# Optimization experiments

Hardware: AMD Instinct MI355X
Metric: run time of the kernel (lower is better)

## Reference

```python
import jax, jax.numpy as jnp
import numpy as np
import math

H = 12  # heads (init kwarg)
KEEP_RATE = 0.7  # forward arg keep_rate (< 1 -> token pruning path)


def setup_inputs() -> dict:
    key = jax.random.key(0)
    k0, k1, k2 = jax.random.split(key, 3)
    b, n, c = 32, 577, 768  # ViT-B/16 @ 384px: 576 patches + CLS
    x = jax.random.normal(k0, (b, n, c), dtype=jnp.float32)
    # nn.Linear(dim, dim*3) and nn.Linear(dim, dim); kaiming-ish scale
    W_qkv = jax.random.normal(k1, (c, 3 * c), dtype=jnp.float32) / np.sqrt(c).astype(np.float32)
    b_qkv = jnp.zeros((3 * c,), dtype=jnp.float32)
    W_out = jax.random.normal(k2, (c, c), dtype=jnp.float32) / np.sqrt(c).astype(np.float32)
    b_out = jnp.zeros((c,), dtype=jnp.float32)
    return {"x": x, "keep_rate": KEEP_RATE, "W_qkv": W_qkv, "b_qkv": b_qkv,
            "W_out": W_out, "b_out": b_out}


def reference(x, keep_rate, W_qkv, b_qkv, W_out, b_out):
    b, n, c = x.shape
    d = c // H
    scale = (c / H) ** -0.5
    # qkv projection + split into heads: 'b n (h d) -> b h n d'
    qkv = x @ W_qkv + b_qkv                      # [b, n, 3c]
    q, k, v = jnp.split(qkv, 3, axis=-1)
    split_heads = lambda t: t.reshape(b, n, H, d).transpose(0, 2, 1, 3)
    q, k, v = split_heads(q), split_heads(k), split_heads(v)
    dots = jnp.einsum('bhid,bhjd->bhij', q, k) * scale   # [b,h,n,n]
    attention = jax.nn.softmax(dots, axis=-1)
    out = jnp.einsum('bhij,bhjd->bhid', attention, v)    # [b,h,n,d]
    out = out.transpose(0, 2, 1, 3).reshape(b, n, c)     # 'b h n d -> b n (h d)'
    out = out @ W_out + b_out                            # to_out (dropout=0)
    final_tokens = n - 1
    if keep_rate < 1:
        final_tokens = math.ceil(keep_rate * final_tokens)
        # CLS-token attention to patch tokens, averaged over heads
        class_attention = attention[:, :, 0, 1:].mean(axis=1)   # [b, n-1]
        _, ind = jax.lax.top_k(class_attention, final_tokens)    # [b, final_tokens]
        ind = jnp.sort(ind, axis=1)
        index = jnp.broadcast_to(ind[:, :, None], (b, final_tokens, c))
        return (x, index, ind, class_attention, final_tokens)
    return (out, None, None, None, final_tokens)
```

## Files before the change

kernel.cpp:

```cpp
#include <hip/hip_runtime.h>
#include <hip/hip_bf16.h>
#include <math.h>

#define BATCH 32
#define NTOK 577
#define NPATCH 576
#define CDIM 768
#define HEADS 12
#define DHEAD 64
#define W3 2304
#define FT 404

#define WS_WTIL  24576
#define WS_DBIAS 319488
#define WS_DOTS  319872
#define WS_IND   541440

#define O_X      0ULL
#define O_INDEX  14180352ULL
#define O_IND    24109056ULL
#define O_CA     24121984ULL
#define O_FT     24140416ULL

__global__ __launch_bounds__(256) void k_fold(const float* __restrict__ x,
                                              const float* __restrict__ W,
                                              const float* __restrict__ bias,
                                              float* __restrict__ wtil,
                                              float* __restrict__ dbias) {
    __shared__ float x0s[CDIM];
    __shared__ float red[256];
    __shared__ float qs[DHEAD];
    const int b = blockIdx.x, h = blockIdx.y, tid = threadIdx.x;
    for (int i = tid; i < CDIM; i += 256) x0s[i] = x[(size_t)b * NTOK * CDIM + i];
    __syncthreads();
    {
        const int d = tid & 63, seg = tid >> 6;
        const float* Wq = W + (size_t)(h * DHEAD + d);
        float acc = 0.f;
        const int c0 = seg * 192;
        #pragma unroll 8
        for (int c = c0; c < c0 + 192; c++)
            acc += x0s[c] * Wq[(size_t)c * W3];
        red[tid] = acc;
    }
    __syncthreads();
    if (tid < DHEAD) {
        float q = red[tid] + red[tid + 64] + red[tid + 128] + red[tid + 192]
                + bias[h * DHEAD + tid];
        qs[tid] = q;
        float t = q * bias[CDIM + h * DHEAD + tid];
        #pragma unroll
        for (int off = 32; off; off >>= 1) t += __shfl_down(t, off);
        if (tid == 0) dbias[b * HEADS + h] = t;
    }
    __syncthreads();
    for (int c = tid; c < CDIM; c += 256) {
        const float* wr = W + (size_t)c * W3 + CDIM + h * DHEAD;
        float acc = 0.f;
        #pragma unroll
        for (int d = 0; d < DHEAD; d += 4) {
            float4 a = *reinterpret_cast<const float4*>(wr + d);
            acc += a.x * qs[d] + a.y * qs[d + 1] + a.z * qs[d + 2] + a.w * qs[d + 3];
        }
        wtil[((size_t)b * HEADS + h) * CDIM + c] = acc;
    }
}

__global__ __launch_bounds__(256) void k_dots(const float* __restrict__ x,
                                              const float* __restrict__ wtil,
                                              const float* __restrict__ dbias,
                                              float* __restrict__ dots,
                                              float* __restrict__ out0) {
    __shared__ float wt[HEADS * CDIM];
    __shared__ float db[HEADS];
    const int b = blockIdx.x, tid = threadIdx.x;
    for (int i = tid; i < HEADS * CDIM; i += 256) wt[i] = wtil[(size_t)b * HEADS * CDIM + i];
    if (tid < HEADS) db[tid] = dbias[b * HEADS + tid];
    __syncthreads();
    const int wave = tid >> 6, lane = tid & 63;
    for (int it = 0; it < 8; it++) {
        const int j = blockIdx.y * 32 + it * 4 + wave;
        if (j >= NTOK) break;
        const float4* xp = reinterpret_cast<const float4*>(x + ((size_t)b * NTOK + j) * CDIM);
        float4* op = reinterpret_cast<float4*>(out0 + ((size_t)b * NTOK + j) * CDIM);
        float acc[HEADS];
        #pragma unroll
        for (int h = 0; h < HEADS; h++) acc[h] = 0.f;
        #pragma unroll
        for (int i = 0; i < 3; i++) {
            float4 a = xp[i * 64 + lane];
            op[i * 64 + lane] = a;
            const int cbase = i * 256 + lane * 4;
            #pragma unroll
            for (int h = 0; h < HEADS; h++) {
                float4 w = *reinterpret_cast<const float4*>(&wt[h * CDIM + cbase]);
                acc[h] += a.x * w.x + a.y * w.y + a.z * w.z + a.w * w.w;
            }
        }
        #pragma unroll
        for (int off = 32; off; off >>= 1)
            #pragma unroll
            for (int h = 0; h < HEADS; h++) acc[h] += __shfl_xor(acc[h], off);
        if (lane == 0) {
            #pragma unroll
            for (int h = 0; h < HEADS; h++)
                dots[((size_t)b * HEADS + h) * NTOK + j] = 0.125f * (acc[h] + db[h]);
        }
    }
}

__global__ __launch_bounds__(768) void k_catopk(const float* __restrict__ dots,
                                                float* __restrict__ ca_out,
                                                float* __restrict__ ind_out,
                                                float* __restrict__ ft_out,
                                                int* __restrict__ ind_ws,
                                                int write_ft) {
    __shared__ float dl[HEADS * NTOK];
    __shared__ float mh[HEADS], sh[HEADS];
    __shared__ unsigned int vals[NPATCH];
    __shared__ int wsum[12];
    const int b = blockIdx.x, tid = threadIdx.x;
    const int w = tid >> 6, lane = tid & 63;
    for (int i = tid; i < HEADS * NTOK; i += 768) dl[i] = dots[(size_t)b * HEADS * NTOK + i];
    __syncthreads();
    {
        const float* row = dl + w * NTOK;
        float m = -3.4e38f;
        for (int j = lane; j < NTOK; j += 64) m = fmaxf(m, row[j]);
        #pragma unroll
        for (int off = 32; off; off >>= 1) m = fmaxf(m, __shfl_xor(m, off));
        float s = 0.f;
        for (int j = lane; j < NTOK; j += 64) s += expf(row[j] - m);
        #pragma unroll
        for (int off = 32; off; off >>= 1) s += __shfl_xor(s, off);
        if (lane == 0) { mh[w] = m; sh[w] = s; }
    }
    __syncthreads();
    unsigned int myv = 0;
    if (tid < NPATCH) {
        float ca = 0.f;
        #pragma unroll
        for (int h = 0; h < HEADS; h++)
            ca += expf(dl[h * NTOK + 1 + tid] - mh[h]) / sh[h];
        ca *= (1.f / 12.f);
        ca_out[(size_t)b * NPATCH + tid] = ca;
        myv = __float_as_uint(ca);
        vals[tid] = myv;
    }
    __syncthreads();
    int f = 0;
    if (tid < NPATCH) {
        int rank = 0;
        const uint4* v4 = reinterpret_cast<const uint4*>(vals);
        #pragma unroll 4
        for (int jb = 0; jb < NPATCH / 4; jb++) {
            const uint4 v = v4[jb];
            const int j = jb * 4;
            rank += (v.x > myv) || (v.x == myv && (j + 0) < tid);
            rank += (v.y > myv) || (v.y == myv && (j + 1) < tid);
            rank += (v.z > myv) || (v.z == myv && (j + 2) < tid);
            rank += (v.w > myv) || (v.w == myv && (j + 3) < tid);
        }
        f = (rank < FT) ? 1 : 0;
    }
    int scan = f;
    #pragma unroll
    for (int off = 1; off < 64; off <<= 1) {
        const int n = __shfl_up(scan, off);
        if (lane >= off) scan += n;
    }
    if (lane == 63) wsum[w] = scan;
    __syncthreads();
    int woff = 0;
    for (int i = 0; i < w; i++) woff += wsum[i];
    if (f) {
        const int pos = woff + scan - 1;
        ind_ws[b * FT + pos] = tid;
        ind_out[(size_t)b * FT + pos] = (float)tid;
    }
    if (b == 0 && tid == 0 && write_ft) ft_out[0] = (float)FT;
}

__global__ __launch_bounds__(256) void k_bcast(const int* __restrict__ ind,
                                               float* __restrict__ out1) {
    const unsigned int g = blockIdx.x * 256u + threadIdx.x;
    const unsigned int e = g * 4u;
    const unsigned int row = e / CDIM;
    const float v = (float)ind[row];
    float4 o; o.x = v; o.y = v; o.z = v; o.w = v;
    *reinterpret_cast<float4*>(out1 + e) = o;
}

extern "C" void kernel_launch(void* const* d_in, const int* in_sizes, int n_in,
                              void* d_out, int out_size, void* d_ws, size_t ws_size,
                              hipStream_t stream) {
    const float* x  = (const float*)d_in[0];
    const float* W  = (const float*)d_in[2];
    const float* bq = (const float*)d_in[3];
    float* ws = (float*)d_ws;
    float* out = (float*)d_out;

    k_fold<<<dim3(BATCH, HEADS), 256, 0, stream>>>(x, W, bq, ws + WS_WTIL, ws + WS_DBIAS);
    k_dots<<<dim3(BATCH, 19), 256, 0, stream>>>(x, ws + WS_WTIL, ws + WS_DBIAS, ws + WS_DOTS, out + O_X);
    const int write_ft = (out_size > (int)O_FT) ? 1 : 0;
    k_catopk<<<BATCH, 768, 0, stream>>>(ws + WS_DOTS, out + O_CA, out + O_IND, out + O_FT,
                                        (int*)(ws + WS_IND), write_ft);
    k_bcast<<<9696, 256, 0, stream>>>((const int*)(ws + WS_IND), out + O_INDEX);
}
```

Baseline: 228.1 us.

## Fuse four kernels into one persistent kernel with grid barriers

Merges the fold, dots, class-attention/top-k and broadcast stages into a single persistent kernel of 512 blocks, separated by atomic-counter grid barriers whose counters are reset with a memset before each launch. This removes three kernel launches and the gaps between them, and the top-k stage now runs with 256 threads, each ranking three patches. In exchange, the fold and top-k phases leave most blocks idle, the final broadcast uses a grid-stride loop, and correctness relies on all 512 blocks being co-resident (two per CU).

```diff
diff --git a/kernel.cpp b/kernel.cpp
--- a/kernel.cpp
+++ b/kernel.cpp
@@ -10,11 +10,13 @@
 #define DHEAD 64
 #define W3 2304
 #define FT 404
+#define GRID 512
 
 #define WS_WTIL  24576
 #define WS_DBIAS 319488
 #define WS_DOTS  319872
 #define WS_IND   541440
+#define WS_BAR   600000
 
 #define O_X      0ULL
 #define O_INDEX  14180352ULL
@@ -22,173 +24,204 @@
 #define O_CA     24121984ULL
 #define O_FT     24140416ULL
 
-__global__ __launch_bounds__(256) void k_fold(const float* __restrict__ x,
-                                              const float* __restrict__ W,
-                                              const float* __restrict__ bias,
-                                              float* __restrict__ wtil,
-                                              float* __restrict__ dbias) {
-    __shared__ float x0s[CDIM];
-    __shared__ float red[256];
-    __shared__ float qs[DHEAD];
-    const int b = blockIdx.x, h = blockIdx.y, tid = threadIdx.x;
-    for (int i = tid; i < CDIM; i += 256) x0s[i] = x[(size_t)b * NTOK * CDIM + i];
+union SmemU {
+    struct { float x0s[CDIM]; float red[256]; float qs[DHEAD]; } p1;
+    struct { float wt[HEADS * CDIM]; float db[HEADS]; } p2;
+    struct { float dl[HEADS * NTOK]; float mh[HEADS]; float sh[HEADS];
+             unsigned int vals[NPATCH]; int wsum[4]; } p3;
+};
+
+__device__ __forceinline__ void grid_barrier(unsigned* ctr) {
     __syncthreads();
+    if (threadIdx.x == 0) {
+        __threadfence();
+        atomicAdd(ctr, 1u);
+        while (__hip_atomic_load(ctr, __ATOMIC_ACQUIRE, __HIP_MEMORY_SCOPE_AGENT) < GRID) {
+            __builtin_amdgcn_s_sleep(1);
+        }
+    }
+    __syncthreads();
+}
+
+__global__ __launch_bounds__(256, 2) void k_all(const float* __restrict__ x,
+                                                const float* __restrict__ W,
+                                                const float* __restrict__ bias,
+                                                float* __restrict__ ws,
+                                                float* __restrict__ out,
+                                                int write_ft) {
+    __shared__ SmemU sm;
+    const int u = blockIdx.x, tid = threadIdx.x;
+    const int w = tid >> 6, lane = tid & 63;
+
+    float* wtil  = ws + WS_WTIL;
+    float* dbias = ws + WS_DBIAS;
+    float* dots  = ws + WS_DOTS;
+    int*   indw  = (int*)(ws + WS_IND);
+    unsigned* bar = (unsigned*)(ws + WS_BAR);
+
+    if (u < BATCH * HEADS) {
+        const int b = u / HEADS, h = u % HEADS;
+        for (int i = tid; i < CDIM; i += 256) sm.p1.x0s[i] = x[(size_t)b * NTOK * CDIM + i];
+        __syncthreads();
+        {
+            const int d = tid & 63, seg = tid >> 6;
+            const float* Wq = W + (size_t)(h * DHEAD + d);
+            float acc = 0.f;
+            const int c0 = seg * 192;
+            #pragma unroll 8
+            for (int c = c0; c < c0 + 192; c++)
+                acc += sm.p1.x0s[c] * Wq[(size_t)c * W3];
+            sm.p1.red[tid] = acc;
+        }
+        __syncthreads();
+        if (tid < DHEAD) {
+            float q = sm.p1.red[tid] + sm.p1.red[tid + 64] + sm.p1.red[tid + 128]
+                    + sm.p1.red[tid + 192] + bias[h * DHEAD + tid];
+            sm.p1.qs[tid] = q;
+            float t = q * bias[CDIM + h * DHEAD + tid];
+            #pragma unroll
+            for (int off = 32; off; off >>= 1) t += __shfl_down(t, off);
+            if (tid == 0) dbias[b * HEADS + h] = t;
+        }
+        __syncthreads();
+        for (int c = tid; c < CDIM; c += 256) {
+            const float* wr = W + (size_t)c * W3 + CDIM + h * DHEAD;
+            float acc = 0.f;
+            #pragma unroll
+            for (int d = 0; d < DHEAD; d += 4) {
+                float4 a = *reinterpret_cast<const float4*>(wr + d);
+                acc += a.x * sm.p1.qs[d] + a.y * sm.p1.qs[d + 1]
+                     + a.z * sm.p1.qs[d + 2] + a.w * sm.p1.qs[d + 3];
+            }
+            wtil[((size_t)b * HEADS + h) * CDIM + c] = acc;
+        }
+    }
+    grid_barrier(bar + 0);
+
     {
-        const int d = tid & 63, seg = tid >> 6;
-        const float* Wq = W + (size_t)(h * DHEAD + d);
-        float acc = 0.f;
-        const int c0 = seg * 192;
-        #pragma unroll 8
-        for (int c = c0; c < c0 + 192; c++)
-            acc += x0s[c] * Wq[(size_t)c * W3];
-        red[tid] = acc;
-    }
-    __syncthreads();
-    if (tid < DHEAD) {
-        float q = red[tid] + red[tid + 64] + red[tid + 128] + red[tid + 192]
-                + bias[h * DHEAD + tid];
-        qs[tid] = q;
-        float t = q * bias[CDIM + h * DHEAD + tid];
+        const int b = u >> 4, c4 = (u & 15) * 4 + w;
+        for (int i = tid; i < HEADS * CDIM; i += 256) sm.p2.wt[i] = wtil[(size_t)b * HEADS * CDIM + i];
+        if (tid < HEADS) sm.p2.db[tid] = dbias[b * HEADS + tid];
+        __syncthreads();
+        for (int it = 0; it < 10; it++) {
+            const int j = it * 64 + c4;
+            if (j >= NTOK) break;
+            const float4* xp = reinterpret_cast<const float4*>(x + ((size_t)b * NTOK + j) * CDIM);
+            float4* op = reinterpret_cast<float4*>(out + O_X + ((size_t)b * NTOK + j) * CDIM);
+            float acc[HEADS];
+            #pragma unroll
+            for (int h = 0; h < HEADS; h++) acc[h] = 0.f;
+            #pragma unroll
+            for (int i = 0; i < 3; i++) {
+                float4 a = xp[i * 64 + lane];
+                op[i * 64 + lane] = a;
+                const int cbase = i * 256 + lane * 4;
+                #pragma unroll
+                for (int h = 0; h < HEADS; h++) {
+                    float4 wv = *reinterpret_cast<const float4*>(&sm.p2.wt[h * CDIM + cbase]);
+                    acc[h] += a.x * wv.x + a.y * wv.y + a.z * wv.z + a.w * wv.w;
+                }
+            }
+            #pragma unroll
+            for (int off = 32; off; off >>= 1)
+                #pragma unroll
+                for (int h = 0; h < HEADS; h++) acc[h] += __shfl_xor(acc[h], off);
+            if (lane == 0) {
+                #pragma unroll
+                for (int h = 0; h < HEADS; h++)
+                    dots[((size_t)b * HEADS + h) * NTOK + j] = 0.125f * (acc[h] + sm.p2.db[h]);
+            }
+        }
+    }
+    grid_barrier(bar + 1);
+
+    if (u < BATCH) {
+        const int b = u;
+        float* dl = sm.p3.dl;
+        for (int i = tid; i < HEADS * NTOK; i += 256) dl[i] = dots[(size_t)b * HEADS * NTOK + i];
+        __syncthreads();
+        for (int hh = 0; hh < 3; hh++) {
+            const int h = w * 3 + hh;
+            const float* row = dl + h * NTOK;
+            float m = -3.4e38f;
+            for (int j = lane; j < NTOK; j += 64) m = fmaxf(m, row[j]);
+            #pragma unroll
+            for (int off = 32; off; off >>= 1) m = fmaxf(m, __shfl_xor(m, off));
+            float s = 0.f;
+            for (int j = lane; j < NTOK; j += 64) s += expf(row[j] - m);
+            #pragma unroll
+            for (int off = 32; off; off >>= 1) s += __shfl_xor(s, off);
+            if (lane == 0) { sm.p3.mh[h] = m; sm.p3.sh[h] = s; }
+        }
+        __syncthreads();
+        for (int p = tid; p < NPATCH; p += 256) {
+            float ca = 0.f;
+            #pragma unroll
+            for (int h = 0; h < HEADS; h++)
+                ca += expf(dl[h * NTOK + 1 + p] - sm.p3.mh[h]) / sm.p3.sh[h];
+            ca *= (1.f / 12.f);
+            out[O_CA + (size_t)b * NPATCH + p] = ca;
+            sm.p3.vals[p] = __float_as_uint(ca);
+        }
+        __syncthreads();
+        int f0 = 0, f1 = 0, f2 = 0;
+        if (tid < 192) {
+            const int p0 = 3 * tid;
+            const unsigned int v0 = sm.p3.vals[p0], v1 = sm.p3.vals[p0 + 1], v2 = sm.p3.vals[p0 + 2];
+            int r0 = 0, r1 = 0, r2 = 0;
+            const uint4* v4 = reinterpret_cast<const uint4*>(sm.p3.vals);
+            #pragma unroll 4
+            for (int jb = 0; jb < NPATCH / 4; jb++) {
+                const uint4 v = v4[jb];
+                const int j = jb * 4;
+                r0 += (v.x > v0) || (v.x == v0 && (j + 0) < p0);
+                r0 += (v.y > v0) || (v.y == v0 && (j + 1) < p0);
+                r0 += (v.z > v0) || (v.z == v0 && (j + 2) < p0);
+                r0 += (v.w > v0) || (v.w == v0 && (j + 3) < p0);
+                r1 += (v.x > v1) || (v.x == v1 && (j + 0) < p0 + 1);
+                r1 += (v.y > v1) || (v.y == v1 && (j + 1) < p0 + 1);
+                r1 += (v.z > v1) || (v.z == v1 && (j + 2) < p0 + 1);
+                r1 += (v.w > v1) || (v.w == v1 && (j + 3) < p0 + 1);
+                r2 += (v.x > v2) || (v.x == v2 && (j + 0) < p0 + 2);
+                r2 += (v.y > v2) || (v.y == v2 && (j + 1) < p0 + 2);
+                r2 += (v.z > v2) || (v.z == v2 && (j + 2) < p0 + 2);
+                r2 += (v.w > v2) || (v.w == v2 && (j + 3) < p0 + 2);
+            }
+            f0 = (r0 < FT) ? 1 : 0;
+            f1 = (r1 < FT) ? 1 : 0;
+            f2 = (r2 < FT) ? 1 : 0;
+        }
+        const int l = f0 + f1 + f2;
+        int scan = l;
         #pragma unroll
-        for (int off = 32; off; off >>= 1) t += __shfl_down(t, off);
-        if (tid == 0) dbias[b * HEADS + h] = t;
-    }
-    __syncthreads();
-    for (int c = tid; c < CDIM; c += 256) {
-        const float* wr = W + (size_t)c * W3 + CDIM + h * DHEAD;
-        float acc = 0.f;
-        #pragma unroll
-        for (int d = 0; d < DHEAD; d += 4) {
-            float4 a = *reinterpret_cast<const float4*>(wr + d);
-            acc += a.x * qs[d] + a.y * qs[d + 1] + a.z * qs[d + 2] + a.w * qs[d + 3];
-        }
-        wtil[((size_t)b * HEADS + h) * CDIM + c] = acc;
-    }
-}
-
-__global__ __launch_bounds__(256) void k_dots(const float* __restrict__ x,
-                                              const float* __restrict__ wtil,
-                                              const float* __restrict__ dbias,
-                                              float* __restrict__ dots,
-                                              float* __restrict__ out0) {
-    __shared__ float wt[HEADS * CDIM];
-    __shared__ float db[HEADS];
-    const int b = blockIdx.x, tid = threadIdx.x;
-    for (int i = tid; i < HEADS * CDIM; i += 256) wt[i] = wtil[(size_t)b * HEADS * CDIM + i];
-    if (tid < HEADS) db[tid] = dbias[b * HEADS + tid];
-    __syncthreads();
-    const int wave = tid >> 6, lane = tid & 63;
-    for (int it = 0; it < 8; it++) {
-        const int j = blockIdx.y * 32 + it * 4 + wave;
-        if (j >= NTOK) break;
-        const float4* xp = reinterpret_cast<const float4*>(x + ((size_t)b * NTOK + j) * CDIM);
-        float4* op = reinterpret_cast<float4*>(out0 + ((size_t)b * NTOK + j) * CDIM);
-        float acc[HEADS];
-        #pragma unroll
-        for (int h = 0; h < HEADS; h++) acc[h] = 0.f;
-        #pragma unroll
-        for (int i = 0; i < 3; i++) {
-            float4 a = xp[i * 64 + lane];
-            op[i * 64 + lane] = a;
-            const int cbase = i * 256 + lane * 4;
-            #pragma unroll
-            for (int h = 0; h < HEADS; h++) {
-                float4 w = *reinterpret_cast<const float4*>(&wt[h * CDIM + cbase]);
-                acc[h] += a.x * w.x + a.y * w.y + a.z * w.z + a.w * w.w;
-            }
-        }
-        #pragma unroll
-        for (int off = 32; off; off >>= 1)
-            #pragma unroll
-            for (int h = 0; h < HEADS; h++) acc[h] += __shfl_xor(acc[h], off);
-        if (lane == 0) {
-            #pragma unroll
-            for (int h = 0; h < HEADS; h++)
-                dots[((size_t)b * HEADS + h) * NTOK + j] = 0.125f * (acc[h] + db[h]);
-        }
-    }
-}
-
-__global__ __launch_bounds__(768) void k_catopk(const float* __restrict__ dots,
-                                                float* __restrict__ ca_out,
-                                                float* __restrict__ ind_out,
-                                                float* __restrict__ ft_out,
-                                                int* __restrict__ ind_ws,
-                                                int write_ft) {
-    __shared__ float dl[HEADS * NTOK];
-    __shared__ float mh[HEADS], sh[HEADS];
-    __shared__ unsigned int vals[NPATCH];
-    __shared__ int wsum[12];
-    const int b = blockIdx.x, tid = threadIdx.x;
-    const int w = tid >> 6, lane = tid & 63;
-    for (int i = tid; i < HEADS * NTOK; i += 768) dl[i] = dots[(size_t)b * HEADS * NTOK + i];
-    __syncthreads();
+        for (int off = 1; off < 64; off <<= 1) {
+            const int n = __shfl_up(scan, off);
+            if (lane >= off) scan += n;
+        }
+        if (lane == 63) sm.p3.wsum[w] = scan;
+        __syncthreads();
+        int woff = 0;
+        for (int i = 0; i < w; i++) woff += sm.p3.wsum[i];
+        if (tid < 192) {
+            int pos = woff + scan - l;
+            const int p0 = 3 * tid;
+            if (f0) { indw[b * FT + pos] = p0;     out[O_IND + (size_t)b * FT + pos] = (float)p0;       pos++; }
+            if (f1) { indw[b * FT + pos] = p0 + 1; out[O_IND + (size_t)b * FT + pos] = (float)(p0 + 1); pos++; }
+            if (f2) { indw[b * FT + pos] = p0 + 2; out[O_IND + (size_t)b * FT + pos] = (float)(p0 + 2); }
+        }
+        if (u == 0 && tid == 0 && write_ft) out[O_FT] = (float)FT;
+    }
+    grid_barrier(bar + 2);
+
     {
-        const float* row = dl + w * NTOK;
-        float m = -3.4e38f;
-        for (int j = lane; j < NTOK; j += 64) m = fmaxf(m, row[j]);
-        #pragma unroll
-        for (int off = 32; off; off >>= 1) m = fmaxf(m, __shfl_xor(m, off));
-        float s = 0.f;
-        for (int j = lane; j < NTOK; j += 64) s += expf(row[j] - m);
-        #pragma unroll
-        for (int off = 32; off; off >>= 1) s += __shfl_xor(s, off);
-        if (lane == 0) { mh[w] = m; sh[w] = s; }
-    }
-    __syncthreads();
-    unsigned int myv = 0;
-    if (tid < NPATCH) {
-        float ca = 0.f;
-        #pragma unroll
-        for (int h = 0; h < HEADS; h++)
-            ca += expf(dl[h * NTOK + 1 + tid] - mh[h]) / sh[h];
-        ca *= (1.f / 12.f);
-        ca_out[(size_t)b * NPATCH + tid] = ca;
-        myv = __float_as_uint(ca);
-        vals[tid] = myv;
-    }
-    __syncthreads();
-    int f = 0;
-    if (tid < NPATCH) {
-        int rank = 0;
-        const uint4* v4 = reinterpret_cast<const uint4*>(vals);
-        #pragma unroll 4
-        for (int jb = 0; jb < NPATCH / 4; jb++) {
-            const uint4 v = v4[jb];
-            const int j = jb * 4;
-            rank += (v.x > myv) || (v.x == myv && (j + 0) < tid);
-            rank += (v.y > myv) || (v.y == myv && (j + 1) < tid);
-            rank += (v.z > myv) || (v.z == myv && (j + 2) < tid);
-            rank += (v.w > myv) || (v.w == myv && (j + 3) < tid);
-        }
-        f = (rank < FT) ? 1 : 0;
-    }
-    int scan = f;
-    #pragma unroll
-    for (int off = 1; off < 64; off <<= 1) {
-        const int n = __shfl_up(scan, off);
-        if (lane >= off) scan += n;
-    }
-    if (lane == 63) wsum[w] = scan;
-    __syncthreads();
-    int woff = 0;
-    for (int i = 0; i < w; i++) woff += wsum[i];
-    if (f) {
-        const int pos = woff + scan - 1;
-        ind_ws[b * FT + pos] = tid;
-        ind_out[(size_t)b * FT + pos] = (float)tid;
-    }
-    if (b == 0 && tid == 0 && write_ft) ft_out[0] = (float)FT;
-}
-
-__global__ __launch_bounds__(256) void k_bcast(const int* __restrict__ ind,
-                                               float* __restrict__ out1) {
-    const unsigned int g = blockIdx.x * 256u + threadIdx.x;
-    const unsigned int e = g * 4u;
-    const unsigned int row = e / CDIM;
-    const float v = (float)ind[row];
-    float4 o; o.x = v; o.y = v; o.z = v; o.w = v;
-    *reinterpret_cast<float4*>(out1 + e) = o;
+        const int nf4 = 2482176;
+        for (int f4 = u * 256 + tid; f4 < nf4; f4 += GRID * 256) {
+            const int row = f4 / 192;
+            const float v = (float)indw[row];
+            float4 o; o.x = v; o.y = v; o.z = v; o.w = v;
+            *reinterpret_cast<float4*>(out + O_INDEX + (size_t)f4 * 4) = o;
+        }
+    }
 }
 
 extern "C" void kernel_launch(void* const* d_in, const int* in_sizes, int n_in,
@@ -199,11 +232,8 @@
     const float* bq = (const float*)d_in[3];
     float* ws = (float*)d_ws;
     float* out = (float*)d_out;
-
-    k_fold<<<dim3(BATCH, HEADS), 256, 0, stream>>>(x, W, bq, ws + WS_WTIL, ws + WS_DBIAS);
-    k_dots<<<dim3(BATCH, 19), 256, 0, stream>>>(x, ws + WS_WTIL, ws + WS_DBIAS, ws + WS_DOTS, out + O_X);
     const int write_ft = (out_size > (int)O_FT) ? 1 : 0;
-    k_catopk<<<BATCH, 768, 0, stream>>>(ws + WS_DOTS, out + O_CA, out + O_IND, out + O_FT,
-                                        (int*)(ws + WS_IND), write_ft);
-    k_bcast<<<9696, 256, 0, stream>>>((const int*)(ws + WS_IND), out + O_INDEX);
+
+    hipMemsetAsync((void*)(ws + WS_BAR), 0, 16, stream);
+    k_all<<<GRID, 256, 0, stream>>>(x, W, bq, ws, out, write_ft);
 }
```

Measured after the change: 516.9 us. 2.27x slower.
